# Optimization experiments

Hardware: AMD Instinct MI355X
Metric: run time of the kernel (lower is better)

Reference implementation:

```python
import jax, jax.numpy as jnp
import numpy as np

COS_EPS = 1e-8  # torch F.cosine_similarity eps


def setup_inputs() -> dict:
    key = jax.random.key(0)
    k1, k2 = jax.random.split(key)
    x = jax.random.normal(k1, (8192, 512), dtype=jnp.float32)
    class_logits = jax.random.normal(k2, (8192, 100), dtype=jnp.float32)
    return {"x": x, "class_logits": class_logits}


def reference(x, class_logits):
    N, D = x.shape
    C = class_logits.shape[1]

    # class_logits.clone().detach()
    logits = jax.lax.stop_gradient(class_logits)
    pred = jax.nn.softmax(logits, axis=1)
    max_logit = pred.max(axis=1)          # [N]
    max_cls = pred.argmax(axis=1)         # [N] int

    # graph(): pairwise cosine similarity = normalize rows + gram matmul
    norms = jnp.linalg.norm(x, axis=1, keepdims=True)
    xn = x / jnp.maximum(norms, COS_EPS)
    mat = xn @ xn.T                       # [N, N]

    x_agg = mat @ x + x                   # [N, D]
    x_new = jax.lax.stop_gradient(x_agg)

    # update_prototype: per-class weighted scatter-add then mean over counts
    weighted = x_new * max_logit[:, None]                     # [N, D]
    sums = jax.ops.segment_sum(weighted, max_cls, num_segments=C)      # [C, D]
    counts = jax.ops.segment_sum(jnp.ones((N,), x.dtype), max_cls, num_segments=C)  # [C]
    prototypes = jnp.where(counts[:, None] > 0,
                           sums / jnp.maximum(counts, 1.0)[:, None],
                           jnp.zeros_like(sums))              # [C, D]

    # inter_class_matrix[i, j] = prototypes[j] - prototypes[i]
    inter_class_matrix = prototypes[None, :, :] - prototypes[:, None, :]  # [C, C, D]
    return prototypes, inter_class_matrix
```

## Files before the change

kernel.cpp:

```cpp
#include <hip/hip_runtime.h>
#include <math.h>

#define N_ROWS 8192
#define D_DIM  512
#define C_CLS  100

typedef unsigned short u16;
typedef unsigned int u32;
typedef __attribute__((ext_vector_type(8))) short short8;
typedef __attribute__((ext_vector_type(4))) float floatx4;

#define WS_G      0
#define WS_INV    262144
#define WS_WV     270336
#define WS_CLS    278528
#define WS_CNT    286720
#define WS_OFFS   286848
#define WS_ORDER  286976
#define WS_U      295168
#define WS_V      346368
#define WS_ZTH    397568
#define WS_ZTL    2494720

#define LDT 65

__device__ __forceinline__ void split2(float v, u16& h, u16& l) {
    unsigned u = __float_as_uint(v);
    h = (u16)(u >> 16);
    float r = v - __uint_as_float(u & 0xFFFF0000u);
    l = (u16)(__float_as_uint(r) >> 16);
}

typedef const __attribute__((address_space(1))) u32* gp32;
typedef __attribute__((address_space(3))) u32* lp32;
__device__ __forceinline__ void cp16(const u16* g, u16* l) {
    __builtin_amdgcn_global_load_lds((gp32)g, (lp32)l, 16, 0, 0);
}

__global__ __launch_bounds__(256) void kA(const float* __restrict__ logits,
        const float* __restrict__ x, float* __restrict__ wv, int* __restrict__ cls,
        float* __restrict__ inv, u16* __restrict__ zth, u16* __restrict__ ztl,
        float* __restrict__ G) {
    __shared__ unsigned zt_p[64 * LDT];
    __shared__ float ns[4][64];
    __shared__ float sv_s[64];
    int bx = blockIdx.x, t = threadIdx.x;
    if (bx < 2048) {
        int row = (bx << 2) + (t >> 6);
        int lane = t & 63;
        const float* lrow = logits + (size_t)row * C_CLS;
        float v1 = lrow[lane];
        bool has2 = (lane + 64) < C_CLS;
        float v2 = has2 ? lrow[lane + 64] : -INFINITY;
        float m; int idx;
        if (v2 > v1) { m = v2; idx = lane + 64; } else { m = v1; idx = lane; }
        #pragma unroll
        for (int off = 32; off >= 1; off >>= 1) {
            float om = __shfl_down(m, off);
            int   oi = __shfl_down(idx, off);
            if (om > m || (om == m && oi < idx)) { m = om; idx = oi; }
        }
        m = __shfl(m, 0);
        idx = __shfl(idx, 0);
        float s = expf(v1 - m) + (has2 ? expf(v2 - m) : 0.0f);
        #pragma unroll
        for (int off = 32; off >= 1; off >>= 1) s += __shfl_down(s, off);
        if (lane == 0) {
            wv[row] = 1.0f / s;
            cls[row] = idx;
        }
        return;
    }
    if (bx >= 2176) {
        int i = ((bx - 2176) * 256 + t) * 32;
        float4 z = make_float4(0.f, 0.f, 0.f, 0.f);
        #pragma unroll
        for (int q = 0; q < 8; ++q) *(float4*)&G[i + q * 4] = z;
        return;
    }
    int r0 = (bx - 2048) << 6;
    {
        int l = t & 63, q = t >> 6;
        const float* src = x + (size_t)(r0 + l) * D_DIM + q * 128;
        float ss = 0.f;
        #pragma unroll
        for (int i = 0; i < 32; ++i) {
            float4 v = *(const float4*)(src + i * 4);
            ss += v.x * v.x + v.y * v.y + v.z * v.z + v.w * v.w;
        }
        ns[q][l] = ss;
    }
    __syncthreads();
    if (t < 64) {
        float ss = ns[0][t] + ns[1][t] + ns[2][t] + ns[3][t];
        float iv = 1.0f / fmaxf(sqrtf(ss), 1e-8f);
        inv[r0 + t] = iv;
        sv_s[t] = sqrtf(iv);
    }
    __syncthreads();
    for (int ct = 0; ct < 8; ++ct) {
        int c0 = ct * 64;
        int r = t >> 2, cq = t & 3;
        const float* src = x + (size_t)(r0 + r) * D_DIM + c0 + cq * 16;
        float vv[16];
        {
            float4 a = *(const float4*)(src + 0);
            float4 b = *(const float4*)(src + 4);
            float4 c = *(const float4*)(src + 8);
            float4 d = *(const float4*)(src + 12);
            vv[0]=a.x; vv[1]=a.y; vv[2]=a.z; vv[3]=a.w;
            vv[4]=b.x; vv[5]=b.y; vv[6]=b.z; vv[7]=b.w;
            vv[8]=c.x; vv[9]=c.y; vv[10]=c.z; vv[11]=c.w;
            vv[12]=d.x; vv[13]=d.y; vv[14]=d.z; vv[15]=d.w;
        }
        float sv = sv_s[r];
        #pragma unroll
        for (int j = 0; j < 16; ++j) {
            u16 h, l;
            split2(sv * vv[j], h, l);
            zt_p[(cq * 16 + j) * LDT + r] = ((unsigned)h << 16) | l;
        }
        __syncthreads();
        int c = t >> 2, rq = (t & 3) * 16;
        size_t tbase = (size_t)(c0 + c) * N_ROWS + r0 + rq;
        uint oh[8], ol[8];
        #pragma unroll
        for (int p = 0; p < 8; ++p) {
            unsigned d0 = zt_p[c * LDT + rq + 2*p];
            unsigned d1 = zt_p[c * LDT + rq + 2*p + 1];
            oh[p] = (d0 >> 16) | (d1 & 0xFFFF0000u);
            ol[p] = (d0 & 0xFFFFu) | (d1 << 16);
        }
        *(uint4*)&zth[tbase]     = make_uint4(oh[0], oh[1], oh[2], oh[3]);
        *(uint4*)&zth[tbase + 8] = make_uint4(oh[4], oh[5], oh[6], oh[7]);
        *(uint4*)&ztl[tbase]     = make_uint4(ol[0], ol[1], ol[2], ol[3]);
        *(uint4*)&ztl[tbase + 8] = make_uint4(ol[4], ol[5], ol[6], ol[7]);
        __syncthreads();
    }
}

__global__ __launch_bounds__(256) void kB(const int* __restrict__ cls,
        int* __restrict__ cnt, int* __restrict__ offs, int* __restrict__ order) {
    __shared__ int hist[128], scan_s[128], cur[128];
    int t = threadIdx.x;
    if (t < 128) hist[t] = 0;
    __syncthreads();
    for (int m = t; m < N_ROWS; m += 256) atomicAdd(&hist[cls[m]], 1);
    __syncthreads();
    if (t < 128) scan_s[t] = hist[t];
    __syncthreads();
    #pragma unroll
    for (int d = 1; d < 128; d <<= 1) {
        int add = (t < 128 && t >= d) ? scan_s[t - d] : 0;
        __syncthreads();
        if (t < 128) scan_s[t] += add;
        __syncthreads();
    }
    if (t < 128) {
        int off0 = scan_s[t] - hist[t];
        cur[t] = off0;
        offs[t] = off0;
        cnt[t] = hist[t];
    }
    __syncthreads();
    for (int m = t; m < N_ROWS; m += 256) {
        int p = atomicAdd(&cur[cls[m]], 1);
        order[p] = m;
    }
}

__global__ __launch_bounds__(256) void kC(const u16* __restrict__ zth,
        const u16* __restrict__ ztl, const float* __restrict__ x,
        const float* __restrict__ inv, const float* __restrict__ wv,
        const int* __restrict__ order, const int* __restrict__ offs,
        const int* __restrict__ cnt, float* __restrict__ G,
        float* __restrict__ u_arr, float* __restrict__ v_arr) {
    __shared__ __attribute__((aligned(16))) union {
        struct { u16 Ah[128*32], Al[128*32], Bh[128*32], Bl[128*32]; } g;
        struct { float us[4][64], vs[4][64]; } uv;
    } sm;
    int bx = blockIdx.x, t = threadIdx.x;
    if (bx >= 160) {
        int idx = bx - 160;
        int c = idx >> 3, jc = idx & 7;
        int g = t >> 6, lane = t & 63;
        int j = jc * 64 + lane;
        int n = cnt[c], o = offs[c];
        float ua = 0.f, va = 0.f;
        for (int p = g; p < n; p += 4) {
            int m = order[o + p];
            float wm = wv[m];
            float wi = wm * inv[m];
            float xv = x[(size_t)m * D_DIM + j];
            ua += wi * xv; va += wm * xv;
        }
        sm.uv.us[g][lane] = ua; sm.uv.vs[g][lane] = va;
        __syncthreads();
        if (g == 0) {
            u_arr[(size_t)c * D_DIM + j] = sm.uv.us[0][lane] + sm.uv.us[1][lane] + sm.uv.us[2][lane] + sm.uv.us[3][lane];
            v_arr[(size_t)c * D_DIM + j] = sm.uv.vs[0][lane] + sm.uv.vs[1][lane] + sm.uv.vs[2][lane] + sm.uv.vs[3][lane];
        }
        return;
    }
    int tile = bx % 10;
    int p = bx / 10;
    int ti = tile < 4 ? 0 : (tile < 7 ? 1 : (tile < 9 ? 2 : 3));
    int tj = tile - (ti == 0 ? 0 : (ti == 1 ? 3 : (ti == 2 ? 5 : 6)));
    int i0 = ti << 7, j0 = tj << 7;
    bool diag = (ti == tj);
    int kb = p << 9;
    int w = t >> 6, l = t & 63;
    int srow = t >> 2, scol = (t & 3) << 3;
    int lm = l & 15, lg = l >> 4;
    floatx4 acc[4][4];
    #pragma unroll
    for (int mi = 0; mi < 4; ++mi)
        #pragma unroll
        for (int ni = 0; ni < 4; ++ni) acc[mi][ni] = (floatx4){0.f,0.f,0.f,0.f};
    int d0 = srow * 32 + scol;
    int d1 = (64 + srow) * 32 + scol;
    const size_t ga0 = (size_t)(i0 + srow) * N_ROWS + kb + scol;
    const size_t ga1 = (size_t)(i0 + 64 + srow) * N_ROWS + kb + scol;
    const size_t gb0 = (size_t)(j0 + srow) * N_ROWS + kb + scol;
    const size_t gb1 = (size_t)(j0 + 64 + srow) * N_ROWS + kb + scol;
    const u16* Bhs = diag ? sm.g.Ah : sm.g.Bh;
    const u16* Bls = diag ? sm.g.Al : sm.g.Bl;
    for (int s = 0; s < 16; ++s) {
        int ks = s << 5;
        cp16(zth + ga0 + ks, sm.g.Ah + d0);
        cp16(zth + ga1 + ks, sm.g.Ah + d1);
        cp16(ztl + ga0 + ks, sm.g.Al + d0);
        cp16(ztl + ga1 + ks, sm.g.Al + d1);
        if (!diag) {
            cp16(zth + gb0 + ks, sm.g.Bh + d0);
            cp16(zth + gb1 + ks, sm.g.Bh + d1);
            cp16(ztl + gb0 + ks, sm.g.Bl + d0);
            cp16(ztl + gb1 + ks, sm.g.Bl + d1);
        }
        __syncthreads();
        short8 ah[4], al[4], bh[4], bl[4];
        #pragma unroll
        for (int mi = 0; mi < 4; ++mi) {
            int off = (((w & 1) << 6) + (mi << 4) + lm) * 32 + (lg << 3);
            ah[mi] = *(const short8*)&sm.g.Ah[off];
            al[mi] = *(const short8*)&sm.g.Al[off];
        }
        #pragma unroll
        for (int ni = 0; ni < 4; ++ni) {
            int off = (((w >> 1) << 6) + (ni << 4) + lm) * 32 + (lg << 3);
            bh[ni] = *(const short8*)&Bhs[off];
            bl[ni] = *(const short8*)&Bls[off];
        }
        #pragma unroll
        for (int mi = 0; mi < 4; ++mi)
            #pragma unroll
            for (int ni = 0; ni < 4; ++ni) {
                acc[mi][ni] = __builtin_amdgcn_mfma_f32_16x16x32_bf16(ah[mi], bh[ni], acc[mi][ni], 0, 0, 0);
                acc[mi][ni] = __builtin_amdgcn_mfma_f32_16x16x32_bf16(ah[mi], bl[ni], acc[mi][ni], 0, 0, 0);
                acc[mi][ni] = __builtin_amdgcn_mfma_f32_16x16x32_bf16(al[mi], bh[ni], acc[mi][ni], 0, 0, 0);
            }
        __syncthreads();
    }
    #pragma unroll
    for (int mi = 0; mi < 4; ++mi) {
        int row0 = i0 + ((w & 1) << 6) + (mi << 4) + (lg << 2);
        #pragma unroll
        for (int ni = 0; ni < 4; ++ni) {
            int col = j0 + ((w >> 1) << 6) + (ni << 4) + lm;
            #pragma unroll
            for (int r = 0; r < 4; ++r) {
                float val = acc[mi][ni][r];
                atomicAdd(&G[(size_t)(row0 + r) * D_DIM + col], val);
                if (!diag)
                    atomicAdd(&G[(size_t)col * D_DIM + (row0 + r)], val);
            }
        }
    }
}

__global__ __launch_bounds__(256) void kD(const float* __restrict__ u_arr,
        const float* __restrict__ v_arr, const int* __restrict__ cnt,
        const float* __restrict__ G, float* __restrict__ out) {
    __shared__ float ug[D_DIM];
    int c = blockIdx.x >> 1;
    int j = ((blockIdx.x & 1) << 8) + threadIdx.x;
    ug[threadIdx.x]       = u_arr[(size_t)c * D_DIM + threadIdx.x];
    ug[threadIdx.x + 256] = u_arr[(size_t)c * D_DIM + threadIdx.x + 256];
    __syncthreads();
    float acc = v_arr[(size_t)c * D_DIM + j];
    #pragma unroll 8
    for (int k = 0; k < D_DIM; ++k)
        acc += ug[k] * G[(size_t)k * D_DIM + j];
    int n = cnt[c];
    float s = (n > 0) ? 1.0f / (float)n : 0.0f;
    out[(size_t)c * D_DIM + j] = acc * s;
}

__global__ __launch_bounds__(256) void kE(const float* __restrict__ proto,
                                          float* __restrict__ inter) {
    int pair = blockIdx.x * 4 + (threadIdx.x >> 6);
    int i = pair / C_CLS;
    int j = pair - i * C_CLS;
    int d = (threadIdx.x & 63) << 3;
    float4 pj0 = *(const float4*)&proto[j * D_DIM + d];
    float4 pj1 = *(const float4*)&proto[j * D_DIM + d + 4];
    float4 pi0 = *(const float4*)&proto[i * D_DIM + d];
    float4 pi1 = *(const float4*)&proto[i * D_DIM + d + 4];
    float4 r0, r1;
    r0.x = pj0.x - pi0.x; r0.y = pj0.y - pi0.y; r0.z = pj0.z - pi0.z; r0.w = pj0.w - pi0.w;
    r1.x = pj1.x - pi1.x; r1.y = pj1.y - pi1.y; r1.z = pj1.z - pi1.z; r1.w = pj1.w - pi1.w;
    *(float4*)&inter[(size_t)pair * D_DIM + d]     = r0;
    *(float4*)&inter[(size_t)pair * D_DIM + d + 4] = r1;
}

extern "C" void kernel_launch(void* const* d_in, const int* in_sizes, int n_in,
                              void* d_out, int out_size, void* d_ws, size_t ws_size,
                              hipStream_t stream) {
    const float* x      = (const float*)d_in[0];
    const float* logits = (const float*)d_in[1];
    float* out = (float*)d_out;
    float* ws  = (float*)d_ws;
    float* G     = ws + WS_G;
    float* inv   = ws + WS_INV;
    float* wv    = ws + WS_WV;
    int*   cls   = (int*)(ws + WS_CLS);
    int*   cnt   = (int*)(ws + WS_CNT);
    int*   offs  = (int*)(ws + WS_OFFS);
    int*   order = (int*)(ws + WS_ORDER);
    float* u_arr = ws + WS_U;
    float* v_arr = ws + WS_V;
    u16* zth = (u16*)(ws + WS_ZTH);
    u16* ztl = (u16*)(ws + WS_ZTL);

    kA<<<2208, 256, 0, stream>>>(logits, x, wv, cls, inv, zth, ztl, G);
    kB<<<1, 256, 0, stream>>>(cls, cnt, offs, order);
    kC<<<960, 256, 0, stream>>>(zth, ztl, x, inv, wv, order, offs, cnt, G, u_arr, v_arr);
    kD<<<C_CLS * 2, 256, 0, stream>>>(u_arr, v_arr, cnt, G, out);
    kE<<<C_CLS * C_CLS / 4, 256, 0, stream>>>(out, out + C_CLS * D_DIM);
}
```

Baseline: 185.6 us.

## Replace split-bf16 three-pass Gram with single fp16 MFMA and restructure prep kernels

Drops the hi/lo bf16 split of the normalized matrix and computes the Gram product with one fp16 MFMA per tile instead of three bf16 MFMAs. This halves the transposed operand storage and the global-to-LDS traffic in kC. kA now stages 32 rows of x in LDS and writes fp16 directly, and kD is re-tiled so each block handles 8 classes by 32 columns, reusing G loads across classes. The cost is accuracy: fp16 has about 11 bits of mantissa versus roughly 16 for the split bf16 scheme, so the result may drift from the fp32 reference.

```diff
diff --git a/kernel.cpp b/kernel.cpp
--- a/kernel.cpp
+++ b/kernel.cpp
@@ -7,7 +7,7 @@
 
 typedef unsigned short u16;
 typedef unsigned int u32;
-typedef __attribute__((ext_vector_type(8))) short short8;
+typedef __attribute__((ext_vector_type(8))) _Float16 half8;
 typedef __attribute__((ext_vector_type(4))) float floatx4;
 
 #define WS_G      0
@@ -20,16 +20,6 @@
 #define WS_U      295168
 #define WS_V      346368
 #define WS_ZTH    397568
-#define WS_ZTL    2494720
-
-#define LDT 65
-
-__device__ __forceinline__ void split2(float v, u16& h, u16& l) {
-    unsigned u = __float_as_uint(v);
-    h = (u16)(u >> 16);
-    float r = v - __uint_as_float(u & 0xFFFF0000u);
-    l = (u16)(__float_as_uint(r) >> 16);
-}
 
 typedef const __attribute__((address_space(1))) u32* gp32;
 typedef __attribute__((address_space(3))) u32* lp32;
@@ -37,105 +27,97 @@
     __builtin_amdgcn_global_load_lds((gp32)g, (lp32)l, 16, 0, 0);
 }
 
+__device__ __forceinline__ u16 f2h(float v) {
+    _Float16 h = (_Float16)v;
+    return *(u16*)&h;
+}
+
 __global__ __launch_bounds__(256) void kA(const float* __restrict__ logits,
         const float* __restrict__ x, float* __restrict__ wv, int* __restrict__ cls,
-        float* __restrict__ inv, u16* __restrict__ zth, u16* __restrict__ ztl,
-        float* __restrict__ G) {
-    __shared__ unsigned zt_p[64 * LDT];
-    __shared__ float ns[4][64];
-    __shared__ float sv_s[64];
+        float* __restrict__ inv, u16* __restrict__ zth, float* __restrict__ G) {
+    __shared__ float xs[32 * 516];
+    __shared__ float ns[8][32];
+    __shared__ float sv_s[32];
     int bx = blockIdx.x, t = threadIdx.x;
-    if (bx < 2048) {
-        int row = (bx << 2) + (t >> 6);
+    if (bx < 1024) {
         int lane = t & 63;
-        const float* lrow = logits + (size_t)row * C_CLS;
-        float v1 = lrow[lane];
-        bool has2 = (lane + 64) < C_CLS;
-        float v2 = has2 ? lrow[lane + 64] : -INFINITY;
-        float m; int idx;
-        if (v2 > v1) { m = v2; idx = lane + 64; } else { m = v1; idx = lane; }
-        #pragma unroll
-        for (int off = 32; off >= 1; off >>= 1) {
-            float om = __shfl_down(m, off);
-            int   oi = __shfl_down(idx, off);
-            if (om > m || (om == m && oi < idx)) { m = om; idx = oi; }
-        }
-        m = __shfl(m, 0);
-        idx = __shfl(idx, 0);
-        float s = expf(v1 - m) + (has2 ? expf(v2 - m) : 0.0f);
-        #pragma unroll
-        for (int off = 32; off >= 1; off >>= 1) s += __shfl_down(s, off);
-        if (lane == 0) {
-            wv[row] = 1.0f / s;
-            cls[row] = idx;
+        int row0 = (bx << 3) + ((t >> 6) << 1);
+        #pragma unroll
+        for (int rr = 0; rr < 2; ++rr) {
+            int row = row0 + rr;
+            const float* lrow = logits + (size_t)row * C_CLS;
+            float v1 = lrow[lane];
+            bool has2 = (lane + 64) < C_CLS;
+            float v2 = has2 ? lrow[lane + 64] : -INFINITY;
+            float m; int idx;
+            if (v2 > v1) { m = v2; idx = lane + 64; } else { m = v1; idx = lane; }
+            #pragma unroll
+            for (int off = 32; off >= 1; off >>= 1) {
+                float om = __shfl_down(m, off);
+                int   oi = __shfl_down(idx, off);
+                if (om > m || (om == m && oi < idx)) { m = om; idx = oi; }
+            }
+            m = __shfl(m, 0);
+            idx = __shfl(idx, 0);
+            float s = expf(v1 - m) + (has2 ? expf(v2 - m) : 0.0f);
+            #pragma unroll
+            for (int off = 32; off >= 1; off >>= 1) s += __shfl_down(s, off);
+            if (lane == 0) {
+                wv[row] = 1.0f / s;
+                cls[row] = idx;
+            }
         }
         return;
     }
-    if (bx >= 2176) {
-        int i = ((bx - 2176) * 256 + t) * 32;
+    if (bx >= 1280) {
+        int i = ((bx - 1280) * 256 + t) * 32;
         float4 z = make_float4(0.f, 0.f, 0.f, 0.f);
         #pragma unroll
         for (int q = 0; q < 8; ++q) *(float4*)&G[i + q * 4] = z;
         return;
     }
-    int r0 = (bx - 2048) << 6;
+    int r0 = (bx - 1024) << 5;
+    const float* src = x + (size_t)r0 * D_DIM;
+    #pragma unroll
+    for (int i = 0; i < 16; ++i) {
+        int e = i * 1024 + t * 4;
+        int r = e >> 9, c = e & 511;
+        *(float4*)&xs[r * 516 + c] = *(const float4*)&src[e];
+    }
+    __syncthreads();
     {
-        int l = t & 63, q = t >> 6;
-        const float* src = x + (size_t)(r0 + l) * D_DIM + q * 128;
+        int r = t & 31, seg = t >> 5;
+        const float* row = &xs[r * 516 + seg * 64];
         float ss = 0.f;
         #pragma unroll
-        for (int i = 0; i < 32; ++i) {
-            float4 v = *(const float4*)(src + i * 4);
-            ss += v.x * v.x + v.y * v.y + v.z * v.z + v.w * v.w;
-        }
-        ns[q][l] = ss;
-    }
-    __syncthreads();
-    if (t < 64) {
-        float ss = ns[0][t] + ns[1][t] + ns[2][t] + ns[3][t];
+        for (int jj = 0; jj < 64; ++jj) { float v = row[jj]; ss += v * v; }
+        ns[seg][r] = ss;
+    }
+    __syncthreads();
+    if (t < 32) {
+        float ss = ns[0][t] + ns[1][t] + ns[2][t] + ns[3][t]
+                 + ns[4][t] + ns[5][t] + ns[6][t] + ns[7][t];
         float iv = 1.0f / fmaxf(sqrtf(ss), 1e-8f);
         inv[r0 + t] = iv;
         sv_s[t] = sqrtf(iv);
     }
     __syncthreads();
+    int c = t >> 2, rq = (t & 3) * 8;
+    float svl[8];
+    #pragma unroll
+    for (int ii = 0; ii < 8; ++ii) svl[ii] = sv_s[rq + ii];
+    #pragma unroll
     for (int ct = 0; ct < 8; ++ct) {
-        int c0 = ct * 64;
-        int r = t >> 2, cq = t & 3;
-        const float* src = x + (size_t)(r0 + r) * D_DIM + c0 + cq * 16;
-        float vv[16];
-        {
-            float4 a = *(const float4*)(src + 0);
-            float4 b = *(const float4*)(src + 4);
-            float4 c = *(const float4*)(src + 8);
-            float4 d = *(const float4*)(src + 12);
-            vv[0]=a.x; vv[1]=a.y; vv[2]=a.z; vv[3]=a.w;
-            vv[4]=b.x; vv[5]=b.y; vv[6]=b.z; vv[7]=b.w;
-            vv[8]=c.x; vv[9]=c.y; vv[10]=c.z; vv[11]=c.w;
-            vv[12]=d.x; vv[13]=d.y; vv[14]=d.z; vv[15]=d.w;
-        }
-        float sv = sv_s[r];
-        #pragma unroll
-        for (int j = 0; j < 16; ++j) {
-            u16 h, l;
-            split2(sv * vv[j], h, l);
-            zt_p[(cq * 16 + j) * LDT + r] = ((unsigned)h << 16) | l;
-        }
-        __syncthreads();
-        int c = t >> 2, rq = (t & 3) * 16;
-        size_t tbase = (size_t)(c0 + c) * N_ROWS + r0 + rq;
-        uint oh[8], ol[8];
-        #pragma unroll
-        for (int p = 0; p < 8; ++p) {
-            unsigned d0 = zt_p[c * LDT + rq + 2*p];
-            unsigned d1 = zt_p[c * LDT + rq + 2*p + 1];
-            oh[p] = (d0 >> 16) | (d1 & 0xFFFF0000u);
-            ol[p] = (d0 & 0xFFFFu) | (d1 << 16);
-        }
-        *(uint4*)&zth[tbase]     = make_uint4(oh[0], oh[1], oh[2], oh[3]);
-        *(uint4*)&zth[tbase + 8] = make_uint4(oh[4], oh[5], oh[6], oh[7]);
-        *(uint4*)&ztl[tbase]     = make_uint4(ol[0], ol[1], ol[2], ol[3]);
-        *(uint4*)&ztl[tbase + 8] = make_uint4(ol[4], ol[5], ol[6], ol[7]);
-        __syncthreads();
+        int d = ct * 64 + c;
+        u16 o[8];
+        #pragma unroll
+        for (int ii = 0; ii < 8; ++ii)
+            o[ii] = f2h(xs[(rq + ii) * 516 + d] * svl[ii]);
+        uint4 val = make_uint4((u32)o[0] | ((u32)o[1] << 16),
+                               (u32)o[2] | ((u32)o[3] << 16),
+                               (u32)o[4] | ((u32)o[5] << 16),
+                               (u32)o[6] | ((u32)o[7] << 16));
+        *(uint4*)&zth[(size_t)d * N_ROWS + r0 + rq] = val;
     }
 }
 
@@ -170,13 +152,12 @@
 }
 
 __global__ __launch_bounds__(256) void kC(const u16* __restrict__ zth,
-        const u16* __restrict__ ztl, const float* __restrict__ x,
-        const float* __restrict__ inv, const float* __restrict__ wv,
-        const int* __restrict__ order, const int* __restrict__ offs,
-        const int* __restrict__ cnt, float* __restrict__ G,
-        float* __restrict__ u_arr, float* __restrict__ v_arr) {
+        const float* __restrict__ x, const float* __restrict__ inv,
+        const float* __restrict__ wv, const int* __restrict__ order,
+        const int* __restrict__ offs, const int* __restrict__ cnt,
+        float* __restrict__ G, float* __restrict__ u_arr, float* __restrict__ v_arr) {
     __shared__ __attribute__((aligned(16))) union {
-        struct { u16 Ah[128*32], Al[128*32], Bh[128*32], Bl[128*32]; } g;
+        struct { u16 Ah[128 * 32], Bh[128 * 32]; } g;
         struct { float us[4][64], vs[4][64]; } uv;
     } sm;
     int bx = blockIdx.x, t = threadIdx.x;
@@ -216,7 +197,7 @@
     #pragma unroll
     for (int mi = 0; mi < 4; ++mi)
         #pragma unroll
-        for (int ni = 0; ni < 4; ++ni) acc[mi][ni] = (floatx4){0.f,0.f,0.f,0.f};
+        for (int ni = 0; ni < 4; ++ni) acc[mi][ni] = (floatx4){0.f, 0.f, 0.f, 0.f};
     int d0 = srow * 32 + scol;
     int d1 = (64 + srow) * 32 + scol;
     const size_t ga0 = (size_t)(i0 + srow) * N_ROWS + kb + scol;
@@ -224,41 +205,31 @@
     const size_t gb0 = (size_t)(j0 + srow) * N_ROWS + kb + scol;
     const size_t gb1 = (size_t)(j0 + 64 + srow) * N_ROWS + kb + scol;
     const u16* Bhs = diag ? sm.g.Ah : sm.g.Bh;
-    const u16* Bls = diag ? sm.g.Al : sm.g.Bl;
     for (int s = 0; s < 16; ++s) {
         int ks = s << 5;
         cp16(zth + ga0 + ks, sm.g.Ah + d0);
         cp16(zth + ga1 + ks, sm.g.Ah + d1);
-        cp16(ztl + ga0 + ks, sm.g.Al + d0);
-        cp16(ztl + ga1 + ks, sm.g.Al + d1);
         if (!diag) {
             cp16(zth + gb0 + ks, sm.g.Bh + d0);
             cp16(zth + gb1 + ks, sm.g.Bh + d1);
-            cp16(ztl + gb0 + ks, sm.g.Bl + d0);
-            cp16(ztl + gb1 + ks, sm.g.Bl + d1);
-        }
-        __syncthreads();
-        short8 ah[4], al[4], bh[4], bl[4];
+        }
+        __syncthreads();
+        half8 ah[4], bh[4];
         #pragma unroll
         for (int mi = 0; mi < 4; ++mi) {
             int off = (((w & 1) << 6) + (mi << 4) + lm) * 32 + (lg << 3);
-            ah[mi] = *(const short8*)&sm.g.Ah[off];
-            al[mi] = *(const short8*)&sm.g.Al[off];
+            ah[mi] = *(const half8*)&sm.g.Ah[off];
         }
         #pragma unroll
         for (int ni = 0; ni < 4; ++ni) {
             int off = (((w >> 1) << 6) + (ni << 4) + lm) * 32 + (lg << 3);
-            bh[ni] = *(const short8*)&Bhs[off];
-            bl[ni] = *(const short8*)&Bls[off];
+            bh[ni] = *(const half8*)&Bhs[off];
         }
         #pragma unroll
         for (int mi = 0; mi < 4; ++mi)
             #pragma unroll
-            for (int ni = 0; ni < 4; ++ni) {
-                acc[mi][ni] = __builtin_amdgcn_mfma_f32_16x16x32_bf16(ah[mi], bh[ni], acc[mi][ni], 0, 0, 0);
-                acc[mi][ni] = __builtin_amdgcn_mfma_f32_16x16x32_bf16(ah[mi], bl[ni], acc[mi][ni], 0, 0, 0);
-                acc[mi][ni] = __builtin_amdgcn_mfma_f32_16x16x32_bf16(al[mi], bh[ni], acc[mi][ni], 0, 0, 0);
-            }
+            for (int ni = 0; ni < 4; ++ni)
+                acc[mi][ni] = __builtin_amdgcn_mfma_f32_16x16x32_f16(ah[mi], bh[ni], acc[mi][ni], 0, 0, 0);
         __syncthreads();
     }
     #pragma unroll
@@ -281,19 +252,28 @@
 __global__ __launch_bounds__(256) void kD(const float* __restrict__ u_arr,
         const float* __restrict__ v_arr, const int* __restrict__ cnt,
         const float* __restrict__ G, float* __restrict__ out) {
-    __shared__ float ug[D_DIM];
-    int c = blockIdx.x >> 1;
-    int j = ((blockIdx.x & 1) << 8) + threadIdx.x;
-    ug[threadIdx.x]       = u_arr[(size_t)c * D_DIM + threadIdx.x];
-    ug[threadIdx.x + 256] = u_arr[(size_t)c * D_DIM + threadIdx.x + 256];
-    __syncthreads();
-    float acc = v_arr[(size_t)c * D_DIM + j];
+    __shared__ float us[8][512];
+    int g = blockIdx.x >> 4;
+    int panel = blockIdx.x & 15;
+    int t = threadIdx.x;
+    for (int idx = t; idx < 8 * 512; idx += 256) {
+        int ci = idx >> 9, k = idx & 511;
+        int cc = g * 8 + ci;
+        us[ci][k] = (cc < C_CLS) ? u_arr[(size_t)cc * D_DIM + k] : 0.f;
+    }
+    __syncthreads();
+    int ci = t >> 5, cj = t & 31;
+    int c = g * 8 + ci;
+    int j = panel * 32 + cj;
+    float acc = 0.f;
     #pragma unroll 8
     for (int k = 0; k < D_DIM; ++k)
-        acc += ug[k] * G[(size_t)k * D_DIM + j];
-    int n = cnt[c];
-    float s = (n > 0) ? 1.0f / (float)n : 0.0f;
-    out[(size_t)c * D_DIM + j] = acc * s;
+        acc += us[ci][k] * G[(size_t)k * D_DIM + j];
+    if (c < C_CLS) {
+        int n = cnt[c];
+        float s = (n > 0) ? 1.0f / (float)n : 0.0f;
+        out[(size_t)c * D_DIM + j] = (v_arr[(size_t)c * D_DIM + j] + acc) * s;
+    }
 }
 
 __global__ __launch_bounds__(256) void kE(const float* __restrict__ proto,
@@ -330,11 +310,10 @@
     float* u_arr = ws + WS_U;
     float* v_arr = ws + WS_V;
     u16* zth = (u16*)(ws + WS_ZTH);
-    u16* ztl = (u16*)(ws + WS_ZTL);
-
-    kA<<<2208, 256, 0, stream>>>(logits, x, wv, cls, inv, zth, ztl, G);
+
+    kA<<<1312, 256, 0, stream>>>(logits, x, wv, cls, inv, zth, G);
     kB<<<1, 256, 0, stream>>>(cls, cnt, offs, order);
-    kC<<<960, 256, 0, stream>>>(zth, ztl, x, inv, wv, order, offs, cnt, G, u_arr, v_arr);
-    kD<<<C_CLS * 2, 256, 0, stream>>>(u_arr, v_arr, cnt, G, out);
+    kC<<<960, 256, 0, stream>>>(zth, x, inv, wv, order, offs, cnt, G, u_arr, v_arr);
+    kD<<<208, 256, 0, stream>>>(u_arr, v_arr, cnt, G, out);
     kE<<<C_CLS * C_CLS / 4, 256, 0, stream>>>(out, out + C_CLS * D_DIM);
 }
```

Measured after the change: 173.1 us. 6.8% less time.
